# Performance work log

Hardware: AMD Instinct MI355X
Metric: run time of the kernel (lower is better)

The kernel has to match this reference:

```python
import jax, jax.numpy as jnp
import numpy as np
import math

E = 1024      # hidden_dim = embed_dim (num_heads=1 so head_dim=E)
ND = 512      # output_dim = asymmetric value dim
N_DOMAIN = 2048
LN_EPS = 1e-5
SCALE = math.sqrt(1.0 / E) * 2.0 * math.log(N_DOMAIN)


def layernorm(x, g, b):
    mu = jnp.mean(x, axis=-1, keepdims=True)
    var = jnp.var(x, axis=-1, keepdims=True)
    return (x - mu) * jax.lax.rsqrt(var + LN_EPS) * g + b


def setup_inputs() -> dict:
    key = jax.random.key(0)
    ks = jax.random.split(key, 5)
    B, L = 8, 2048
    return {
        "x": jax.random.normal(ks[0], (B, L, E), dtype=jnp.float32),
        "in_proj_w": jax.random.normal(ks[1], (2 * E + ND, E), dtype=jnp.float32) * 0.02,
        "w1": jax.random.normal(ks[2], (2048, ND), dtype=jnp.float32) * 0.02,
        "b1": jnp.zeros((2048,), dtype=jnp.float32),
        "w2": jax.random.normal(ks[3], (ND, 2048), dtype=jnp.float32) * 0.02,
        "b2": jnp.zeros((ND,), dtype=jnp.float32),
        "g1": jnp.ones((ND,), dtype=jnp.float32),
        "be1": jnp.zeros((ND,), dtype=jnp.float32),
        "g2": jnp.ones((ND,), dtype=jnp.float32),
        "be2": jnp.zeros((ND,), dtype=jnp.float32),
    }


def reference(x, in_proj_w, w1, b1, w2, b2, g1, be1, g2, be2):
    # fused in-projection (no bias): q,k get E dims, v gets ND dims
    proj = jnp.einsum("ble,fe->blf", x, in_proj_w)
    q = proj[..., :E]
    k = proj[..., E:2 * E]
    v = proj[..., 2 * E:]
    # custom scale: sqrt(1/head_dim) * 2 * log(N)
    scores = jnp.einsum("bld,bsd->bls", q * SCALE, k)  # [B, L, S]
    attn_w = jax.nn.softmax(scores, axis=-1)
    attn_out = jnp.einsum("bls,bsd->bld", attn_w, v)   # [B, L, ND] (no out proj)
    # skip=False (hidden_dim != output_dim): norm1(attn) only
    h = layernorm(attn_out, g1, be1)
    ff = jnp.einsum("bld,fd->blf", h, w1) + b1
    ff = jnp.einsum("blf,df->bld", jax.nn.relu(ff), w2) + b2
    return layernorm(h + ff, g2, be2)
```

## Files before the change

kernel.cpp:

```cpp
#include <hip/hip_runtime.h>
#include <hip/hip_bf16.h>

typedef unsigned short u16;
typedef unsigned int u32;
typedef float f32x4 __attribute__((ext_vector_type(4)));
typedef _Float16 f16x8 __attribute__((ext_vector_type(8)));
typedef u32 u32x4 __attribute__((ext_vector_type(4)));
typedef u32 u32x2 __attribute__((ext_vector_type(2)));

#define SEQ 2048
#define EDIM 1024

__device__ __forceinline__ u16 f2h(float f) {
  _Float16 h = (_Float16)f;
  return __builtin_bit_cast(u16, h);
}
__device__ __forceinline__ float h2f(u16 u) {
  return (float)__builtin_bit_cast(_Float16, u);
}
__device__ __forceinline__ u32 pk(float a, float b) {
  return (u32)f2h(a) | ((u32)f2h(b) << 16);
}

#define N_X  2097152
#define N_WP 327680
#define N_W1 131072
#define N_W2 131072
__global__ __launch_bounds__(256) void cvt_all(const float* __restrict__ x, u16* __restrict__ xb,
                                               const float* __restrict__ wp, u16* __restrict__ wpb,
                                               const float* __restrict__ w1, u16* __restrict__ w1b,
                                               const float* __restrict__ w2, u16* __restrict__ w2b) {
  int i = blockIdx.x * 256 + threadIdx.x;
  const float* src; u16* dst; int li;
  if (i < N_X) { src = x; dst = xb; li = i; }
  else if (i < N_X + N_WP) { src = wp; dst = wpb; li = i - N_X; }
  else if (i < N_X + N_WP + N_W1) { src = w1; dst = w1b; li = i - N_X - N_WP; }
  else if (i < N_X + N_WP + N_W1 + N_W2) { src = w2; dst = w2b; li = i - N_X - N_WP - N_W1; }
  else return;
  const f32x4* p = (const f32x4*)(src + (size_t)li * 8);
  f32x4 a = p[0], b = p[1];
  u32x4 o = {pk(a[0], a[1]), pk(a[2], a[3]), pk(b[0], b[1]), pk(b[2], b[3])};
  *(u32x4*)(dst + (size_t)li * 8) = o;
}

struct GemmP {
  const u16* A; const u16* B;
  int lda, ldb, K;
  long bsA, bsB, bsC;
  int ldc;
  u16* Cb;
  const float* bias;
  const u16* resid;
  u16* qk; u16* vT;
  float scale;
};

template <int EPI>
__global__ __launch_bounds__(256) void gemm_bt(GemmP p) {
  __shared__ __align__(16) char lds[65536];
  const int tid = threadIdx.x;
  const int lane = tid & 63;
  const int wave = tid >> 6;
  const int wm = wave >> 1, wn = wave & 1;
  const int bn0 = blockIdx.x * 128;
  const int bm0 = blockIdx.y * 128;
  const int z = blockIdx.z;

  const u16* gA[4]; const u16* gB[4];
  int ldsA[4], ldsB[4];
  {
    const u16* Ab = p.A + (long)z * p.bsA + (long)bm0 * p.lda;
    const u16* Bb = p.B + (long)z * p.bsB + (long)bn0 * p.ldb;
#pragma unroll
    for (int i = 0; i < 4; ++i) {
      int ch = i * 256 + tid;
      int row = ch >> 3, s = ch & 7;
      int ks = ((s ^ (row & 7)) << 3);
      gA[i] = Ab + (long)row * p.lda + ks;
      gB[i] = Bb + (long)row * p.ldb + ks;
      ldsA[i] = ch * 16;
      ldsB[i] = 16384 + ch * 16;
    }
  }
  auto stage = [&](int buf) {
    char* dst = lds + buf * 32768;
#pragma unroll
    for (int i = 0; i < 4; ++i) {
      __builtin_amdgcn_global_load_lds(
          (const __attribute__((address_space(1))) u32*)gA[i],
          (__attribute__((address_space(3))) u32*)(dst + ldsA[i]), 16, 0, 0);
      gA[i] += 64;
    }
#pragma unroll
    for (int i = 0; i < 4; ++i) {
      __builtin_amdgcn_global_load_lds(
          (const __attribute__((address_space(1))) u32*)gB[i],
          (__attribute__((address_space(3))) u32*)(dst + ldsB[i]), 16, 0, 0);
      gB[i] += 64;
    }
  };

  int ao[2][4], bo[2][4];
#pragma unroll
  for (int h = 0; h < 2; ++h) {
#pragma unroll
    for (int i = 0; i < 4; ++i) {
      int rA = wm * 64 + i * 16 + (lane & 15);
      ao[h][i] = rA * 128 + ((((h << 2) | (lane >> 4)) ^ (rA & 7)) << 4);
      int rB = wn * 64 + i * 16 + (lane & 15);
      bo[h][i] = 16384 + rB * 128 + ((((h << 2) | (lane >> 4)) ^ (rB & 7)) << 4);
    }
  }

  f32x4 acc[4][4] = {};
  stage(0);
  const int nk = p.K >> 6;
  int cur = 0;
  for (int kt = 0; kt < nk; ++kt) {
    __syncthreads();
    if (kt + 1 < nk) stage(cur ^ 1);
    const char* base = lds + cur * 32768;
#pragma unroll
    for (int h = 0; h < 2; ++h) {
      f16x8 av[4], bv[4];
#pragma unroll
      for (int i = 0; i < 4; ++i) av[i] = *(const f16x8*)(base + ao[h][i]);
#pragma unroll
      for (int j = 0; j < 4; ++j) bv[j] = *(const f16x8*)(base + bo[h][j]);
#pragma unroll
      for (int i = 0; i < 4; ++i)
#pragma unroll
        for (int j = 0; j < 4; ++j)
          acc[i][j] = __builtin_amdgcn_mfma_f32_16x16x32_f16(av[i], bv[j], acc[i][j], 0, 0, 0);
    }
    cur ^= 1;
  }

#pragma unroll
  for (int i = 0; i < 4; ++i) {
#pragma unroll
    for (int j = 0; j < 4; ++j) {
      int mb = bm0 + wm * 64 + i * 16 + ((lane >> 4) << 2);
      int n = bn0 + wn * 64 + j * 16 + (lane & 15);
      if constexpr (EPI == 1) {
        int b = mb >> 11, l0 = mb & 2047;
        if (n < EDIM) {
          u16* dst = p.qk + (long)b * 4194304 + (long)l0 * 1024 + n;
#pragma unroll
          for (int r = 0; r < 4; ++r) dst[r * 1024] = f2h(acc[i][j][r] * p.scale);
        } else if (n < 2 * EDIM) {
          u16* dst = p.qk + (long)b * 4194304 + 2097152 + (long)l0 * 1024 + (n - EDIM);
#pragma unroll
          for (int r = 0; r < 4; ++r) dst[r * 1024] = f2h(acc[i][j][r]);
        } else {
          u16* dst = p.vT + (long)b * 1048576 + (long)(n - 2 * EDIM) * 2048 + l0;
          u32x2 w = {pk(acc[i][j][0], acc[i][j][1]), pk(acc[i][j][2], acc[i][j][3])};
          *(u32x2*)dst = w;
        }
      } else if constexpr (EPI == 2) {
        u16* dst = p.Cb + (long)mb * p.ldc + n;
        float bias = p.bias[n];
#pragma unroll
        for (int r = 0; r < 4; ++r) dst[(long)r * p.ldc] = f2h(fmaxf(acc[i][j][r] + bias, 0.f));
      } else if constexpr (EPI == 3) {
        float bias = p.bias[n];
        u16* dst = p.Cb + (long)mb * 512 + n;
        const u16* rs = p.resid + (long)mb * 512 + n;
#pragma unroll
        for (int r = 0; r < 4; ++r) dst[r * 512] = f2h(acc[i][j][r] + bias + h2f(rs[r * 512]));
      } else {
        u16* dst = p.Cb + (long)z * p.bsC + (long)mb * p.ldc + n;
#pragma unroll
        for (int r = 0; r < 4; ++r) dst[(long)r * p.ldc] = f2h(acc[i][j][r]);
      }
    }
  }
}

__global__ __launch_bounds__(256) void softmax_rows(const u16* __restrict__ S,
                                                    u16* __restrict__ W, int b0) {
  int r = blockIdx.x;
  int z = r >> 11, l = r & 2047;
  int tid = threadIdx.x, lane = tid & 63, wv = tid >> 6;
  const u16* x = S + (long)r * 2048 + tid * 8;
  u32x4 raw = *(const u32x4*)x;
  float e[8];
#pragma unroll
  for (int q = 0; q < 4; ++q) {
    e[2 * q] = h2f((u16)(raw[q] & 0xffff));
    e[2 * q + 1] = h2f((u16)(raw[q] >> 16));
  }
  float m = e[0];
#pragma unroll
  for (int q = 1; q < 8; ++q) m = fmaxf(m, e[q]);
#pragma unroll
  for (int off = 32; off; off >>= 1) m = fmaxf(m, __shfl_xor(m, off));
  __shared__ float red[8];
  if (lane == 0) red[wv] = m;
  __syncthreads();
  m = fmaxf(fmaxf(red[0], red[1]), fmaxf(red[2], red[3]));
  float s = 0.f;
#pragma unroll
  for (int q = 0; q < 8; ++q) { e[q] = __expf(e[q] - m); s += e[q]; }
#pragma unroll
  for (int off = 32; off; off >>= 1) s += __shfl_xor(s, off);
  if (lane == 0) red[4 + wv] = s;
  __syncthreads();
  s = red[4] + red[5] + red[6] + red[7];
  float inv = 1.f / s;
  u32x4 o = {pk(e[0] * inv, e[1] * inv), pk(e[2] * inv, e[3] * inv),
             pk(e[4] * inv, e[5] * inv), pk(e[6] * inv, e[7] * inv)};
  *(u32x4*)(W + (long)(b0 + z) * 4194304 + (long)l * 2048 + tid * 8) = o;
}

template <int INF16, int OUTF16>
__global__ __launch_bounds__(256) void ln_rows(const void* __restrict__ X,
                                               const float* __restrict__ g,
                                               const float* __restrict__ bb,
                                               void* __restrict__ out) {
  int row = blockIdx.x * 4 + (threadIdx.x >> 6);
  int lane = threadIdx.x & 63;
  float v[8];
  if constexpr (INF16) {
    u32x4 raw = *(const u32x4*)((const u16*)X + (long)row * 512 + lane * 8);
#pragma unroll
    for (int q = 0; q < 4; ++q) {
      v[2 * q] = h2f((u16)(raw[q] & 0xffff));
      v[2 * q + 1] = h2f((u16)(raw[q] >> 16));
    }
  } else {
    const float* x = (const float*)X + (long)row * 512 + lane * 8;
    f32x4 a = *(const f32x4*)x, b = *(const f32x4*)(x + 4);
#pragma unroll
    for (int q = 0; q < 4; ++q) { v[q] = a[q]; v[4 + q] = b[q]; }
  }
  float s = 0.f, sq = 0.f;
#pragma unroll
  for (int q = 0; q < 8; ++q) { s += v[q]; sq += v[q] * v[q]; }
#pragma unroll
  for (int off = 32; off; off >>= 1) {
    s += __shfl_xor(s, off);
    sq += __shfl_xor(sq, off);
  }
  float mean = s * (1.f / 512.f);
  float var = sq * (1.f / 512.f) - mean * mean;
  float rstd = rsqrtf(var + 1e-5f);
  f32x4 g0 = *(const f32x4*)(g + lane * 8), g1v = *(const f32x4*)(g + lane * 8 + 4);
  f32x4 b0 = *(const f32x4*)(bb + lane * 8), b1v = *(const f32x4*)(bb + lane * 8 + 4);
  float o[8];
#pragma unroll
  for (int q = 0; q < 4; ++q) o[q] = (v[q] - mean) * rstd * g0[q] + b0[q];
#pragma unroll
  for (int q = 0; q < 4; ++q) o[4 + q] = (v[4 + q] - mean) * rstd * g1v[q] + b1v[q];
  if constexpr (OUTF16) {
    u32x4 pkd = {pk(o[0], o[1]), pk(o[2], o[3]), pk(o[4], o[5]), pk(o[6], o[7])};
    *(u32x4*)((u16*)out + (long)row * 512 + lane * 8) = pkd;
  } else {
    float* dst = (float*)out + (long)row * 512 + lane * 8;
    *(f32x4*)dst = (f32x4){o[0], o[1], o[2], o[3]};
    *(f32x4*)(dst + 4) = (f32x4){o[4], o[5], o[6], o[7]};
  }
}

extern "C" void kernel_launch(void* const* d_in, const int* in_sizes, int n_in,
                              void* d_out, int out_size, void* d_ws, size_t ws_size,
                              hipStream_t stream) {
  const float* x = (const float*)d_in[0];
  const float* wp = (const float*)d_in[1];
  const float* w1 = (const float*)d_in[2];
  const float* b1 = (const float*)d_in[3];
  const float* w2 = (const float*)d_in[4];
  const float* b2 = (const float*)d_in[5];
  const float* g1 = (const float*)d_in[6];
  const float* be1 = (const float*)d_in[7];
  const float* g2 = (const float*)d_in[8];
  const float* be2 = (const float*)d_in[9];

  char* ws = (char*)d_ws;
  size_t off = 0;
  auto alloc = [&](size_t bytes) {
    char* p = ws + off;
    off += (bytes + 255) & ~(size_t)255;
    return p;
  };
  u16* wpb = (u16*)alloc(2560 * 1024 * 2);
  u16* w1b = (u16*)alloc(2048 * 512 * 2);
  u16* w2b = (u16*)alloc(512 * 2048 * 2);
  char* xb_region = alloc(33554432);
  u16* qk = (u16*)alloc(67108864);
  u16* vT = (u16*)alloc(16777216);
  u16* hb = (u16*)alloc(16777216);
  int bpl = (ws_size >= off + (size_t)67108864) ? 8 : 4;
  char* sc_region = alloc((size_t)bpl * 2048 * 2048 * 2);
  if (off > ws_size) return;

  u16* xb = (u16*)xb_region;
  u16* attn16 = (u16*)xb_region;
  u16* scores = (u16*)sc_region;
  u16* y16 = (u16*)sc_region;
  u16* ff1 = qk;

  const float SC = (float)(0.03125 * 2.0 * 7.6246189861593985);

  cvt_all<<<dim3(10496), dim3(256), 0, stream>>>(x, xb, wp, wpb, w1, w1b, w2, w2b);

  {
    GemmP p{};
    p.A = xb; p.lda = 1024; p.B = wpb; p.ldb = 1024; p.K = 1024;
    p.qk = qk; p.vT = vT; p.scale = SC;
    gemm_bt<1><<<dim3(20, 128, 1), 256, 0, stream>>>(p);
  }

  for (int it = 0; it < 8 / bpl; ++it) {
    int b0 = it * bpl;
    GemmP p{};
    p.A = qk + (long)b0 * 4194304; p.lda = 1024; p.bsA = 4194304;
    p.B = qk + (long)b0 * 4194304 + 2097152; p.ldb = 1024; p.bsB = 4194304;
    p.K = 1024; p.Cb = scores; p.ldc = 2048; p.bsC = 4194304;
    gemm_bt<4><<<dim3(16, 16, bpl), 256, 0, stream>>>(p);
    softmax_rows<<<dim3(bpl * 2048), dim3(256), 0, stream>>>(scores, qk, b0);
  }

  {
    GemmP p{};
    p.A = qk; p.lda = 2048; p.bsA = 4194304;
    p.B = vT; p.ldb = 2048; p.bsB = 1048576;
    p.K = 2048; p.Cb = attn16; p.ldc = 512; p.bsC = 1048576;
    gemm_bt<4><<<dim3(4, 16, 8), 256, 0, stream>>>(p);
  }

  ln_rows<1, 1><<<dim3(4096), dim3(256), 0, stream>>>(attn16, g1, be1, hb);

  {
    GemmP p{};
    p.A = hb; p.lda = 512; p.B = w1b; p.ldb = 512; p.K = 512;
    p.Cb = ff1; p.ldc = 2048; p.bias = b1;
    gemm_bt<2><<<dim3(16, 128, 1), 256, 0, stream>>>(p);
  }

  {
    GemmP p{};
    p.A = ff1; p.lda = 2048; p.B = w2b; p.ldb = 2048; p.K = 2048;
    p.Cb = y16; p.bias = b2; p.resid = hb;
    gemm_bt<3><<<dim3(4, 128, 1), 256, 0, stream>>>(p);
  }

  ln_rows<1, 0><<<dim3(4096), dim3(256), 0, stream>>>(y16, g2, be2, (float*)d_out);
}
```

Baseline: 379.1 us.

## Add 256x256-tile 8-wave GEMM kernel for projection, scores and FF1

```diff
diff --git a/kernel.cpp b/kernel.cpp
--- a/kernel.cpp
+++ b/kernel.cpp
@@ -56,6 +56,122 @@
 };
 
 template <int EPI>
+__global__ __launch_bounds__(512, 2) void gemm256(GemmP p) {
+  __shared__ __align__(16) char lds[131072];
+  const int tid = threadIdx.x;
+  const int lane = tid & 63;
+  const int wave = tid >> 6;
+  const int wm = wave >> 2, wn = wave & 3;
+  const int bn0 = blockIdx.x * 256;
+  const int bm0 = blockIdx.y * 256;
+  const int z = blockIdx.z;
+
+  const u16* gA[4]; const u16* gB[4];
+  int ldsA[4], ldsB[4];
+  {
+    const u16* Ab = p.A + (long)z * p.bsA + (long)bm0 * p.lda;
+    const u16* Bb = p.B + (long)z * p.bsB + (long)bn0 * p.ldb;
+#pragma unroll
+    for (int i = 0; i < 4; ++i) {
+      int ch = i * 512 + tid;
+      int row = ch >> 3, s = ch & 7;
+      int ks = ((s ^ (row & 7)) << 3);
+      gA[i] = Ab + (long)row * p.lda + ks;
+      gB[i] = Bb + (long)row * p.ldb + ks;
+      ldsA[i] = ch * 16;
+      ldsB[i] = 32768 + ch * 16;
+    }
+  }
+  auto stage = [&](int buf) {
+    char* dst = lds + buf * 65536;
+#pragma unroll
+    for (int i = 0; i < 4; ++i) {
+      __builtin_amdgcn_global_load_lds(
+          (const __attribute__((address_space(1))) u32*)gA[i],
+          (__attribute__((address_space(3))) u32*)(dst + ldsA[i]), 16, 0, 0);
+      gA[i] += 64;
+    }
+#pragma unroll
+    for (int i = 0; i < 4; ++i) {
+      __builtin_amdgcn_global_load_lds(
+          (const __attribute__((address_space(1))) u32*)gB[i],
+          (__attribute__((address_space(3))) u32*)(dst + ldsB[i]), 16, 0, 0);
+      gB[i] += 64;
+    }
+  };
+
+  int abase[2], bbase[2];
+  {
+    int rA = wm * 128 + (lane & 15);
+    int sA = (lane >> 4) ^ (lane & 7);
+    abase[0] = rA * 128 + (sA << 4);
+    abase[1] = abase[0] ^ 64;
+    int rB = wn * 64 + (lane & 15);
+    int sB = (lane >> 4) ^ (lane & 7);
+    bbase[0] = 32768 + rB * 128 + (sB << 4);
+    bbase[1] = bbase[0] ^ 64;
+  }
+
+  f32x4 acc[8][4] = {};
+  stage(0);
+  const int nk = p.K >> 6;
+  int cur = 0;
+  for (int kt = 0; kt < nk; ++kt) {
+    __syncthreads();
+    if (kt + 1 < nk) stage(cur ^ 1);
+    const char* base = lds + cur * 65536;
+#pragma unroll
+    for (int h = 0; h < 2; ++h) {
+      f16x8 av[8], bv[4];
+#pragma unroll
+      for (int m = 0; m < 8; ++m) av[m] = *(const f16x8*)(base + abase[h] + m * 2048);
+#pragma unroll
+      for (int j = 0; j < 4; ++j) bv[j] = *(const f16x8*)(base + bbase[h] + j * 2048);
+#pragma unroll
+      for (int m = 0; m < 8; ++m)
+#pragma unroll
+        for (int j = 0; j < 4; ++j)
+          acc[m][j] = __builtin_amdgcn_mfma_f32_16x16x32_f16(av[m], bv[j], acc[m][j], 0, 0, 0);
+    }
+    cur ^= 1;
+  }
+
+#pragma unroll
+  for (int i = 0; i < 8; ++i) {
+#pragma unroll
+    for (int j = 0; j < 4; ++j) {
+      int mb = bm0 + wm * 128 + i * 16 + ((lane >> 4) << 2);
+      int n = bn0 + wn * 64 + j * 16 + (lane & 15);
+      if constexpr (EPI == 1) {
+        int b = mb >> 11, l0 = mb & 2047;
+        if (n < EDIM) {
+          u16* dst = p.qk + (long)b * 4194304 + (long)l0 * 1024 + n;
+#pragma unroll
+          for (int r = 0; r < 4; ++r) dst[r * 1024] = f2h(acc[i][j][r] * p.scale);
+        } else if (n < 2 * EDIM) {
+          u16* dst = p.qk + (long)b * 4194304 + 2097152 + (long)l0 * 1024 + (n - EDIM);
+#pragma unroll
+          for (int r = 0; r < 4; ++r) dst[r * 1024] = f2h(acc[i][j][r]);
+        } else {
+          u16* dst = p.vT + (long)b * 1048576 + (long)(n - 2 * EDIM) * 2048 + l0;
+          u32x2 w = {pk(acc[i][j][0], acc[i][j][1]), pk(acc[i][j][2], acc[i][j][3])};
+          *(u32x2*)dst = w;
+        }
+      } else if constexpr (EPI == 2) {
+        u16* dst = p.Cb + (long)mb * p.ldc + n;
+        float bias = p.bias[n];
+#pragma unroll
+        for (int r = 0; r < 4; ++r) dst[(long)r * p.ldc] = f2h(fmaxf(acc[i][j][r] + bias, 0.f));
+      } else {
+        u16* dst = p.Cb + (long)z * p.bsC + (long)mb * p.ldc + n;
+#pragma unroll
+        for (int r = 0; r < 4; ++r) dst[(long)r * p.ldc] = f2h(acc[i][j][r]);
+      }
+    }
+  }
+}
+
+template <int EPI>
 __global__ __launch_bounds__(256) void gemm_bt(GemmP p) {
   __shared__ __align__(16) char lds[65536];
   const int tid = threadIdx.x;
@@ -142,27 +258,7 @@
     for (int j = 0; j < 4; ++j) {
       int mb = bm0 + wm * 64 + i * 16 + ((lane >> 4) << 2);
       int n = bn0 + wn * 64 + j * 16 + (lane & 15);
-      if constexpr (EPI == 1) {
-        int b = mb >> 11, l0 = mb & 2047;
-        if (n < EDIM) {
-          u16* dst = p.qk + (long)b * 4194304 + (long)l0 * 1024 + n;
-#pragma unroll
-          for (int r = 0; r < 4; ++r) dst[r * 1024] = f2h(acc[i][j][r] * p.scale);
-        } else if (n < 2 * EDIM) {
-          u16* dst = p.qk + (long)b * 4194304 + 2097152 + (long)l0 * 1024 + (n - EDIM);
-#pragma unroll
-          for (int r = 0; r < 4; ++r) dst[r * 1024] = f2h(acc[i][j][r]);
-        } else {
-          u16* dst = p.vT + (long)b * 1048576 + (long)(n - 2 * EDIM) * 2048 + l0;
-          u32x2 w = {pk(acc[i][j][0], acc[i][j][1]), pk(acc[i][j][2], acc[i][j][3])};
-          *(u32x2*)dst = w;
-        }
-      } else if constexpr (EPI == 2) {
-        u16* dst = p.Cb + (long)mb * p.ldc + n;
-        float bias = p.bias[n];
-#pragma unroll
-        for (int r = 0; r < 4; ++r) dst[(long)r * p.ldc] = f2h(fmaxf(acc[i][j][r] + bias, 0.f));
-      } else if constexpr (EPI == 3) {
+      if constexpr (EPI == 3) {
         float bias = p.bias[n];
         u16* dst = p.Cb + (long)mb * 512 + n;
         const u16* rs = p.resid + (long)mb * 512 + n;
@@ -308,7 +404,7 @@
     GemmP p{};
     p.A = xb; p.lda = 1024; p.B = wpb; p.ldb = 1024; p.K = 1024;
     p.qk = qk; p.vT = vT; p.scale = SC;
-    gemm_bt<1><<<dim3(20, 128, 1), 256, 0, stream>>>(p);
+    gemm256<1><<<dim3(10, 64, 1), 512, 0, stream>>>(p);
   }
 
   for (int it = 0; it < 8 / bpl; ++it) {
@@ -317,7 +413,7 @@
     p.A = qk + (long)b0 * 4194304; p.lda = 1024; p.bsA = 4194304;
     p.B = qk + (long)b0 * 4194304 + 2097152; p.ldb = 1024; p.bsB = 4194304;
     p.K = 1024; p.Cb = scores; p.ldc = 2048; p.bsC = 4194304;
-    gemm_bt<4><<<dim3(16, 16, bpl), 256, 0, stream>>>(p);
+    gemm256<4><<<dim3(8, 8, bpl), 512, 0, stream>>>(p);
     softmax_rows<<<dim3(bpl * 2048), dim3(256), 0, stream>>>(scores, qk, b0);
   }
 
@@ -335,7 +431,7 @@
     GemmP p{};
     p.A = hb; p.lda = 512; p.B = w1b; p.ldb = 512; p.K = 512;
     p.Cb = ff1; p.ldc = 2048; p.bias = b1;
-    gemm_bt<2><<<dim3(16, 128, 1), 256, 0, stream>>>(p);
+    gemm256<2><<<dim3(8, 64, 1), 512, 0, stream>>>(p);
   }
 
   {
```

Result: no change. 376.5 us (-0.7%).
